# Optimization experiments

Hardware: AMD Instinct MI355X
Metric: run time of the kernel (lower is better)

## Reference

```python
import jax, jax.numpy as jnp
import numpy as np

B, T, C = 1, 2048, 1024
H = 16
HD = C // H  # 64
K = 8
EPS = 1e-6
NEG = -1.0e9


def apply_rotary_emb(x, cos, sin):
    # x: (B,T,H,HD), cos/sin: (T, HD//2)
    x1, x2 = jnp.split(x, 2, axis=-1)
    c = cos[None, :, None, :]
    s = sin[None, :, None, :]
    return jnp.concatenate([x1 * c - x2 * s, x1 * s + x2 * c], axis=-1)


def rms_norm(x):
    return x * jax.lax.rsqrt(jnp.mean(jnp.square(x), axis=-1, keepdims=True) + EPS)


def setup_inputs() -> dict:
    key = jax.random.key(0)
    ks = jax.random.split(key, 8)
    x = jax.random.normal(ks[0], (B, T, C), dtype=jnp.float32)
    # standard RoPE tables
    inv_freq = 1.0 / (10000.0 ** (np.arange(0, HD, 2, dtype=np.float32) / HD))
    t = np.arange(T, dtype=np.float32)
    freqs = np.outer(t, inv_freq)  # (T, HD//2)
    cos = jnp.asarray(np.cos(freqs), dtype=jnp.float32)
    sin = jnp.asarray(np.sin(freqs), dtype=jnp.float32)
    std = 0.02
    Wq = std * jax.random.normal(ks[1], (C, C), dtype=jnp.float32)
    Wk = std * jax.random.normal(ks[2], (C, C), dtype=jnp.float32)
    Wv = std * jax.random.normal(ks[3], (C, C), dtype=jnp.float32)
    Wproj = std * jax.random.normal(ks[4], (C, C), dtype=jnp.float32)
    Wdq = jax.random.normal(ks[5], (C, K), dtype=jnp.float32) / np.sqrt(C)
    Wdk = jax.random.normal(ks[6], (C, K), dtype=jnp.float32) / np.sqrt(C)
    return {"x": x, "cos": cos, "sin": sin, "Wq": Wq, "Wk": Wk, "Wv": Wv,
            "Wproj": Wproj, "Wdq": Wdq, "Wdk": Wdk}


def reference(x, cos, sin, Wq, Wk, Wv, Wproj, Wdq, Wdk):
    b, t, c = x.shape
    q = (x @ Wq).reshape(b, t, H, HD)
    k = (x @ Wk).reshape(b, t, H, HD)
    v = (x @ Wv).reshape(b, t, H, HD)
    q = rms_norm(apply_rotary_emb(q, cos, sin))
    k = rms_norm(apply_rotary_emb(k, cos, sin))

    # digit projections (identical for every head in the source module)
    qd = x @ Wdq  # (B,T,K)
    kd = x @ Wdk  # (B,T,K)
    matches = qd[:, :, None, :] == kd[:, None, :, :]  # (B,Tq,Tk,K)
    prefix = jnp.cumprod(matches.astype(jnp.int32), axis=-1)
    lcp = jnp.sum(prefix, axis=-1)  # (B,Tq,Tk)
    lcp_mask = lcp >= (K - 1)

    causal = jnp.tril(jnp.ones((t, t), dtype=bool))
    combined = causal[None, None, :, :] & lcp_mask[:, None, :, :]  # (B,1->H,Tq,Tk)

    scale = 1.0 / jnp.sqrt(jnp.asarray(HD, x.dtype))
    scores = jnp.einsum('bqhd,bkhd->bhqk', q * scale, k)
    scores = jnp.where(combined, scores, NEG)
    w = jax.nn.softmax(scores, axis=-1)
    y = jnp.einsum('bhqk,bkhd->bqhd', w, v).reshape(b, t, c)
    return y @ Wproj
```

## Files before the change

kernel.cpp:

```cpp
#include <hip/hip_runtime.h>
#include <math.h>

#define T_DIM 2048
#define C_DIM 1024
#define H_NUM 16
#define HD_DIM 64
#define K_LCP 8
#define NEG_VAL -1.0e9f

typedef __bf16 bf16;
typedef __bf16 bf16x4 __attribute__((ext_vector_type(4)));
typedef __bf16 bf16x8 __attribute__((ext_vector_type(8)));
typedef float f32x4 __attribute__((ext_vector_type(4)));

__global__ __launch_bounds__(256) void convert_qdkd(const float* __restrict__ x,
                                                    const float* __restrict__ Wdq,
                                                    const float* __restrict__ Wdk,
                                                    bf16* __restrict__ xb,
                                                    float* __restrict__ qd,
                                                    float* __restrict__ kd) {
  const int wave = threadIdx.x >> 6, lane = threadIdx.x & 63;
  const int t = blockIdx.x * 4 + wave;
  const float* xp = x + (size_t)t * C_DIM;
  bf16* xbp = xb + (size_t)t * C_DIM;
  float aq[8] = {}, ak[8] = {};
#pragma unroll
  for (int i = 0; i < 16; ++i) {
    const int c = i * 64 + lane;
    float xv = xp[c];
    xbp[c] = (bf16)xv;
    float4 wq0 = *(const float4*)(Wdq + (size_t)c * K_LCP);
    float4 wq1 = *(const float4*)(Wdq + (size_t)c * K_LCP + 4);
    float4 wk0 = *(const float4*)(Wdk + (size_t)c * K_LCP);
    float4 wk1 = *(const float4*)(Wdk + (size_t)c * K_LCP + 4);
    aq[0] = fmaf(xv, wq0.x, aq[0]); aq[1] = fmaf(xv, wq0.y, aq[1]);
    aq[2] = fmaf(xv, wq0.z, aq[2]); aq[3] = fmaf(xv, wq0.w, aq[3]);
    aq[4] = fmaf(xv, wq1.x, aq[4]); aq[5] = fmaf(xv, wq1.y, aq[5]);
    aq[6] = fmaf(xv, wq1.z, aq[6]); aq[7] = fmaf(xv, wq1.w, aq[7]);
    ak[0] = fmaf(xv, wk0.x, ak[0]); ak[1] = fmaf(xv, wk0.y, ak[1]);
    ak[2] = fmaf(xv, wk0.z, ak[2]); ak[3] = fmaf(xv, wk0.w, ak[3]);
    ak[4] = fmaf(xv, wk1.x, ak[4]); ak[5] = fmaf(xv, wk1.y, ak[5]);
    ak[6] = fmaf(xv, wk1.z, ak[6]); ak[7] = fmaf(xv, wk1.w, ak[7]);
  }
#pragma unroll
  for (int j = 0; j < 8; ++j) {
#pragma unroll
    for (int off = 32; off >= 1; off >>= 1) {
      aq[j] += __shfl_xor(aq[j], off);
      ak[j] += __shfl_xor(ak[j], off);
    }
  }
  if (lane == 0) {
    *(float4*)(qd + (size_t)t * K_LCP) = make_float4(aq[0], aq[1], aq[2], aq[3]);
    *(float4*)(qd + (size_t)t * K_LCP + 4) = make_float4(aq[4], aq[5], aq[6], aq[7]);
    *(float4*)(kd + (size_t)t * K_LCP) = make_float4(ak[0], ak[1], ak[2], ak[3]);
    *(float4*)(kd + (size_t)t * K_LCP + 4) = make_float4(ak[4], ak[5], ak[6], ak[7]);
  }
}

__global__ __launch_bounds__(256) void tilemask_fused(
    const float* __restrict__ qd, const float* __restrict__ kd,
    const float* __restrict__ x, int* __restrict__ tilemask,
    int* __restrict__ allmask, float* __restrict__ partial) {
  const int tid = threadIdx.x;
  if (blockIdx.x >= 128) {
    const int b = blockIdx.x - 128;
    f32x4 s = {0.f, 0.f, 0.f, 0.f};
    for (int r = 0; r < 64; ++r)
      s += ((const f32x4*)(x + (size_t)(b * 64 + r) * C_DIM))[tid];
    ((f32x4*)(partial + (size_t)b * C_DIM))[tid] = s;
    return;
  }
  const int qb = blockIdx.x;
  __shared__ float qds[16][K_LCP];
  __shared__ int tm[32];
  if (tid < 32) tm[tid] = 0;
  if (tid < 16 * K_LCP)
    qds[tid >> 3][tid & 7] = qd[(size_t)(qb * 16 + (tid >> 3)) * K_LCP + (tid & 7)];
  __syncthreads();
  for (int key = tid; key < T_DIM; key += 256) {
    float kv[K_LCP];
    *(float4*)&kv[0] = *(const float4*)(kd + (size_t)key * K_LCP);
    *(float4*)&kv[4] = *(const float4*)(kd + (size_t)key * K_LCP + 4);
    int any = 0;
#pragma unroll
    for (int ql = 0; ql < 16; ++ql) {
      int qg = qb * 16 + ql;
      if (key > qg) continue;
      int lcp = 0;
#pragma unroll
      for (int jj = 0; jj < K_LCP; ++jj) {
        if (qds[ql][jj] == kv[jj]) lcp++;
        else break;
      }
      if (lcp >= K_LCP - 1) any = 1;
    }
    if (any) tm[key >> 6] = 1;
  }
  __syncthreads();
  if (tid < 32) tilemask[qb * 32 + tid] = tm[tid];
  if (tid == 0) {
    int any = 0;
#pragma unroll
    for (int i = 0; i < 32; ++i) any |= tm[i];
    allmask[qb] = !any;
  }
}

__global__ __launch_bounds__(256) void matvec_kernel(
    const float* __restrict__ vin, int npart, const float* __restrict__ W,
    float* __restrict__ vout, float scale, const int* __restrict__ tilemask,
    const int* __restrict__ allmask, int* __restrict__ qneed,
    int* __restrict__ kneed, int* __restrict__ vneed, int* __restrict__ vtneed,
    int* __restrict__ pneed, int* __restrict__ wneed, int do_need) {
  __shared__ float xm[C_DIM];
  __shared__ float red[4][64];
  const int t = threadIdx.x;
  f32x4 s = {0.f, 0.f, 0.f, 0.f};
  if (npart) {
    for (int g = 0; g < npart; ++g) s += ((const f32x4*)vin)[g * 256 + t];
  } else {
    s = ((const f32x4*)vin)[t];
  }
  s *= scale;
  *(f32x4*)&xm[t * 4] = s;
  __syncthreads();
  const int j = blockIdx.x * 64 + (t & 63);
  const int p = t >> 6;
  float acc = 0.f;
  for (int c = p * 256; c < p * 256 + 256; ++c)
    acc = fmaf(xm[c], W[(size_t)c * C_DIM + j], acc);
  red[p][t & 63] = acc;
  __syncthreads();
  if (t < 64)
    vout[blockIdx.x * 64 + t] = (red[0][t] + red[1][t]) + (red[2][t] + red[3][t]);

  if (do_need && blockIdx.x == 0) {
    __shared__ int tmor[32], vt[32], am[128], qn[16], kn[16], vn[16], pn[32];
    if (t < 128) am[t] = allmask[t];
    __syncthreads();
    if (t < 32) {
      int o = 0, v = 0;
      for (int qb = 0; qb < T_DIM / 16; ++qb) {
        int tm = tilemask[qb * 32 + t];
        o |= tm;
        v |= ((!am[qb]) && (!tm));
      }
      tmor[t] = o;
      vt[t] = v;
      vtneed[t] = v;
    }
    __syncthreads();
    if (t < 16) {
      int kn_ = tmor[2 * t] | tmor[2 * t + 1];
      kn[t] = kn_;
      kneed[t] = kn_;
      int q = 0;
#pragma unroll
      for (int jj = 0; jj < 8; ++jj) q |= !am[t * 8 + jj];
      qn[t] = q;
      qneed[t] = q;
      int v_ = kn_ | vt[2 * t] | vt[2 * t + 1];
      vn[t] = v_;
      vneed[t] = v_;
    }
    if (t >= 32 && t < 64) {
      int i = t - 32, pp = 0;
#pragma unroll
      for (int jj = 0; jj < 4; ++jj) pp |= !am[i * 4 + jj];
      pn[i] = pp;
      pneed[i] = pp;
    }
    __syncthreads();
    if (t == 0) {
      int a = 0, b = 0, c = 0, d = 0;
      for (int i = 0; i < 16; ++i) { a |= qn[i]; b |= kn[i]; c |= vn[i]; }
      for (int i = 0; i < 32; ++i) d |= pn[i];
      wneed[0] = a; wneed[1] = b; wneed[2] = c; wneed[3] = d;
    }
  }
}

__global__ __launch_bounds__(256) void transpose_w(const float* __restrict__ W0,
                                                   const float* __restrict__ W1,
                                                   const float* __restrict__ W2,
                                                   const float* __restrict__ W3,
                                                   bf16* __restrict__ O0,
                                                   bf16* __restrict__ O1,
                                                   bf16* __restrict__ O2,
                                                   bf16* __restrict__ O3,
                                                   const int* __restrict__ wneed) {
  if (!wneed[blockIdx.z]) return;
  const float* W = (blockIdx.z == 0) ? W0 : (blockIdx.z == 1) ? W1
                   : (blockIdx.z == 2) ? W2 : W3;
  bf16* O = (blockIdx.z == 0) ? O0 : (blockIdx.z == 1) ? O1
            : (blockIdx.z == 2) ? O2 : O3;
  __shared__ bf16 tile[64][65];
  const int bk = blockIdx.y * 64;
  const int bn = blockIdx.x * 64;
  const int r = threadIdx.x >> 2;
  const int c0 = (threadIdx.x & 3) * 16;
  const float* src = W + (size_t)(bk + r) * C_DIM + bn + c0;
#pragma unroll
  for (int t = 0; t < 16; t += 4) {
    float4 f = *(const float4*)(src + t);
    tile[r][c0 + t + 0] = (bf16)f.x;
    tile[r][c0 + t + 1] = (bf16)f.y;
    tile[r][c0 + t + 2] = (bf16)f.z;
    tile[r][c0 + t + 3] = (bf16)f.w;
  }
  __syncthreads();
  bf16* dst = O + (size_t)(bn + r) * C_DIM + bk + c0;
#pragma unroll
  for (int t = 0; t < 16; ++t) dst[t] = tile[c0 + t][r];
}

template <int TMt, int MI, int NA>
__global__ __launch_bounds__(256) void gemm_bf16(
    const bf16* __restrict__ A, const bf16* __restrict__ Bt0,
    const bf16* __restrict__ Bt1, const bf16* __restrict__ Bt2, void* C0,
    void* C1, void* C2, int N, int Kd, int bf16_out,
    const float* __restrict__ cosT, const float* __restrict__ sinT,
    const int* __restrict__ fq, const int* __restrict__ fk,
    const int* __restrict__ fv, float* __restrict__ vtsum, int mode) {
  if (mode) {
    const int* f = (blockIdx.z == 0) ? fq : (blockIdx.z == 1) ? fk : fv;
    if (!f[blockIdx.y]) return;
  } else {
    if (!fq[blockIdx.y]) return;
  }
  const bf16* Bt = (blockIdx.z == 0) ? Bt0 : (blockIdx.z == 1) ? Bt1 : Bt2;
  __shared__ __align__(16) bf16 As[TMt * 32];
  __shared__ __align__(16) bf16 Bs[128 * 32];
  const int tid = threadIdx.x;
  const int bm = blockIdx.y * TMt;
  const int bn = blockIdx.x * 128;
  const int wave = tid >> 6, lane = tid & 63;
  const int lr = lane >> 2;
  const int lc = (lane & 3) * 8;
  bf16* gA = (bf16*)(A + (size_t)(bm + wave * 16 * NA + lr) * Kd + lc);
  bf16* gB = (bf16*)(Bt + (size_t)(bn + wave * 32 + lr) * Kd + lc);
  bf16* lA = As + wave * 512 * NA;
  bf16* lB = Bs + wave * 1024;
  const int wr = (wave >> 1) * (MI * 16);
  const int wc = (wave & 1) * 64;
  const int fm = lane & 15;
  const int fk_ = (lane >> 4) * 8;

  f32x4 acc[MI][4] = {};
  for (int k0 = 0; k0 < Kd; k0 += 32) {
    __syncthreads();
#pragma unroll
    for (int u = 0; u < NA; ++u)
      __builtin_amdgcn_global_load_lds(
          (__attribute__((address_space(1))) void*)(gA + (size_t)u * 16 * Kd + k0),
          (__attribute__((address_space(3))) void*)(lA + u * 512), 16, 0, 0);
#pragma unroll
    for (int u = 0; u < 2; ++u)
      __builtin_amdgcn_global_load_lds(
          (__attribute__((address_space(1))) void*)(gB + (size_t)u * 16 * Kd + k0),
          (__attribute__((address_space(3))) void*)(lB + u * 512), 16, 0, 0);
    __syncthreads();
    bf16x8 af[MI], bfr[4];
#pragma unroll
    for (int i = 0; i < MI; ++i)
      af[i] = *(const bf16x8*)(As + (size_t)(wr + i * 16 + fm) * 32 + fk_);
#pragma unroll
    for (int j = 0; j < 4; ++j)
      bfr[j] = *(const bf16x8*)(Bs + (size_t)(wc + j * 16 + fm) * 32 + fk_);
#pragma unroll
    for (int i = 0; i < MI; ++i)
#pragma unroll
      for (int j = 0; j < 4; ++j)
        acc[i][j] = __builtin_amdgcn_mfma_f32_16x16x32_bf16(af[i], bfr[j],
                                                            acc[i][j], 0, 0, 0);
  }
  const int cq = (lane >> 4) * 4;
  if (mode && blockIdx.z < 2) {
    bf16* C = (bf16*)((blockIdx.z == 0) ? C0 : C1);
#pragma unroll
    for (int i = 0; i < MI; ++i)
#pragma unroll
      for (int r = 0; r < 4; ++r) {
        const int t = bm + wr + i * 16 + cq + r;
        float c0 = cosT[(size_t)t * 32 + fm], s0 = sinT[(size_t)t * 32 + fm];
        float c1 = cosT[(size_t)t * 32 + 16 + fm], s1 = sinT[(size_t)t * 32 + 16 + fm];
        float a0 = acc[i][0][r], a1 = acc[i][1][r];
        float a2 = acc[i][2][r], a3 = acc[i][3][r];
        float o0 = a0 * c0 - a2 * s0, o2 = a0 * s0 + a2 * c0;
        float o1 = a1 * c1 - a3 * s1, o3 = a1 * s1 + a3 * c1;
        float ss = o0 * o0 + o1 * o1 + o2 * o2 + o3 * o3;
        ss += __shfl_xor(ss, 1);
        ss += __shfl_xor(ss, 2);
        ss += __shfl_xor(ss, 4);
        ss += __shfl_xor(ss, 8);
        float rn = 1.0f / sqrtf(ss * (1.0f / 64.0f) + 1e-6f);
        size_t base = (size_t)t * N + bn + wc + fm;
        C[base + 0] = (bf16)(o0 * rn);
        C[base + 16] = (bf16)(o1 * rn);
        C[base + 32] = (bf16)(o2 * rn);
        C[base + 48] = (bf16)(o3 * rn);
      }
  } else if (bf16_out) {
    bf16* C = (bf16*)((blockIdx.z == 0) ? C0 : (blockIdx.z == 1) ? C1 : C2);
#pragma unroll
    for (int i = 0; i < MI; ++i)
#pragma unroll
      for (int r = 0; r < 4; ++r) {
        size_t base = (size_t)(bm + wr + i * 16 + cq + r) * N + bn + wc + fm;
#pragma unroll
        for (int j = 0; j < 4; ++j) C[base + j * 16] = (bf16)acc[i][j][r];
      }
    if (mode && blockIdx.z == 2 && MI == 4) {
      const int kt = (bm + wr) >> 6;
#pragma unroll
      for (int j = 0; j < 4; ++j) {
        float s = 0.f;
#pragma unroll
        for (int i = 0; i < MI; ++i)
#pragma unroll
          for (int r = 0; r < 4; ++r) s += acc[i][j][r];
        s += __shfl_xor(s, 16);
        s += __shfl_xor(s, 32);
        if ((lane >> 4) == 0)
          vtsum[(size_t)kt * C_DIM + bn + wc + j * 16 + fm] = s;
      }
    }
  } else {
    float* C = (float*)((blockIdx.z == 0) ? C0 : (blockIdx.z == 1) ? C1 : C2);
#pragma unroll
    for (int i = 0; i < MI; ++i)
#pragma unroll
      for (int r = 0; r < 4; ++r) {
        size_t base = (size_t)(bm + wr + i * 16 + cq + r) * N + bn + wc + fm;
#pragma unroll
        for (int j = 0; j < 4; ++j) C[base + j * 16] = acc[i][j][r];
      }
  }
}

#define QT 16
#define KT 64

__global__ __launch_bounds__(256) void attn2(
    const bf16* __restrict__ q, const bf16* __restrict__ k,
    const bf16* __restrict__ v, const float* __restrict__ qd,
    const float* __restrict__ kd, const float* __restrict__ vtsum,
    const float* __restrict__ vmean, const int* __restrict__ tilemask,
    const int* __restrict__ allmask, const int* __restrict__ pneed,
    bf16* __restrict__ y) {
  const int h = blockIdx.y;
  const int qb = blockIdx.x;
  const int q0 = qb * QT;
  const int tid = threadIdx.x;
  const int q_l = tid >> 4;
  const int sub = tid & 15;

  if (allmask[qb]) {
    if (pneed[qb >> 2]) {
      f32x4 vm = *(const f32x4*)(vmean + h * HD_DIM + sub * 4);
      bf16x4 o = {(bf16)vm[0], (bf16)vm[1], (bf16)vm[2], (bf16)vm[3]};
      *(bf16x4*)(y + (size_t)(q0 + q_l) * C_DIM + h * HD_DIM + sub * 4) = o;
    }
    return;
  }

  __shared__ float qs[QT][HD_DIM];
  __shared__ float qds[QT][K_LCP];
  __shared__ float ks[KT][HD_DIM];
  __shared__ float vs[KT][HD_DIM];
  __shared__ float kds[KT][K_LCP];
  __shared__ float sc[QT][KT + 4];

  {
    int r = tid >> 4, c4 = (tid & 15) * 4;
    bf16x4 t4 = *(const bf16x4*)(q + (size_t)(q0 + r) * C_DIM + h * HD_DIM + c4);
    qs[r][c4 + 0] = (float)t4[0] * 0.125f;
    qs[r][c4 + 1] = (float)t4[1] * 0.125f;
    qs[r][c4 + 2] = (float)t4[2] * 0.125f;
    qs[r][c4 + 3] = (float)t4[3] * 0.125f;
    if (tid < QT * K_LCP)
      qds[tid >> 3][tid & 7] = qd[(size_t)(q0 + (tid >> 3)) * K_LCP + (tid & 7)];
  }
  __syncthreads();

  float m = -INFINITY;
  float l = 0.f;
  float acc[4] = {0.f, 0.f, 0.f, 0.f};

  for (int kt = 0; kt < T_DIM / KT; ++kt) {
    if (!tilemask[qb * 32 + kt]) {
      if (m <= NEG_VAL) {
        m = NEG_VAL;
        l += (float)KT;
        f32x4 vt = *(const f32x4*)(vtsum + (size_t)kt * C_DIM + h * HD_DIM + sub * 4);
        acc[0] += vt[0];
        acc[1] += vt[1];
        acc[2] += vt[2];
        acc[3] += vt[3];
      }
      continue;
    }
    const int k0 = kt * KT;
    __syncthreads();
#pragma unroll
    for (int it = 0; it < 4; ++it) {
      int i = tid + it * 256;
      int row = i >> 4, c4 = (i & 15) * 4;
      bf16x4 kv = *(const bf16x4*)(k + (size_t)(k0 + row) * C_DIM + h * HD_DIM + c4);
      bf16x4 vv = *(const bf16x4*)(v + (size_t)(k0 + row) * C_DIM + h * HD_DIM + c4);
      ks[row][c4 + 0] = (float)kv[0];
      ks[row][c4 + 1] = (float)kv[1];
      ks[row][c4 + 2] = (float)kv[2];
      ks[row][c4 + 3] = (float)kv[3];
      vs[row][c4 + 0] = (float)vv[0];
      vs[row][c4 + 1] = (float)vv[1];
      vs[row][c4 + 2] = (float)vv[2];
      vs[row][c4 + 3] = (float)vv[3];
    }
#pragma unroll
    for (int it = 0; it < 2; ++it) {
      int i = tid + it * 256;
      kds[i >> 3][i & 7] = kd[(size_t)(k0 + (i >> 3)) * K_LCP + (i & 7)];
    }
    __syncthreads();

    const int kb = sub * 4;
    bool msk[4];
#pragma unroll
    for (int j = 0; j < 4; ++j) {
      int kg = k0 + kb + j;
      int lcp = 0;
#pragma unroll
      for (int jj = 0; jj < K_LCP; ++jj) {
        if (qds[q_l][jj] == kds[kb + j][jj]) lcp++;
        else break;
      }
      msk[j] = (lcp >= K_LCP - 1) && (kg <= q0 + q_l);
    }
    float s[4] = {0.f, 0.f, 0.f, 0.f};
#pragma unroll
    for (int d4 = 0; d4 < 16; ++d4) {
      float4 q4 = *(const float4*)&qs[q_l][d4 * 4];
#pragma unroll
      for (int j = 0; j < 4; ++j) {
        float4 k4 = *(const float4*)&ks[kb + j][d4 * 4];
        s[j] = fmaf(q4.x, k4.x, s[j]);
        s[j] = fmaf(q4.y, k4.y, s[j]);
        s[j] = fmaf(q4.z, k4.z, s[j]);
        s[j] = fmaf(q4.w, k4.w, s[j]);
      }
    }
    float tmax = NEG_VAL;
#pragma unroll
    for (int j = 0; j < 4; ++j) {
      s[j] = msk[j] ? s[j] : NEG_VAL;
      tmax = fmaxf(tmax, s[j]);
    }
#pragma unroll
    for (int off = 1; off < 16; off <<= 1) tmax = fmaxf(tmax, __shfl_xor(tmax, off));
    float m_new = fmaxf(m, tmax);
    float alpha = expf(m - m_new);
    float lsum = 0.f;
#pragma unroll
    for (int j = 0; j < 4; ++j) {
      float p = expf(s[j] - m_new);
      sc[q_l][kb + j] = p;
      lsum += p;
    }
#pragma unroll
    for (int off = 1; off < 16; off <<= 1) lsum += __shfl_xor(lsum, off);
    l = l * alpha + lsum;
    m = m_new;
    acc[0] *= alpha;
    acc[1] *= alpha;
    acc[2] *= alpha;
    acc[3] *= alpha;
    __syncthreads();
#pragma unroll 8
    for (int kk = 0; kk < KT; ++kk) {
      float w = sc[q_l][kk];
      const float4 v4 = *(const float4*)&vs[kk][sub * 4];
      acc[0] = fmaf(w, v4.x, acc[0]);
      acc[1] = fmaf(w, v4.y, acc[1]);
      acc[2] = fmaf(w, v4.z, acc[2]);
      acc[3] = fmaf(w, v4.w, acc[3]);
    }
  }

  const float inv_l = 1.0f / l;
  bf16x4 o = {(bf16)(acc[0] * inv_l), (bf16)(acc[1] * inv_l),
              (bf16)(acc[2] * inv_l), (bf16)(acc[3] * inv_l)};
  *(bf16x4*)(y + (size_t)(q0 + q_l) * C_DIM + h * HD_DIM + sub * 4) = o;
}

__global__ __launch_bounds__(256) void bcast_out(const float* __restrict__ rowout,
                                                 const int* __restrict__ pneed,
                                                 float* __restrict__ out) {
  f32x4 v = ((const f32x4*)rowout)[threadIdx.x];
  const int r0 = blockIdx.x * 8;
#pragma unroll
  for (int r = 0; r < 8; ++r) {
    const int row = r0 + r;
    if (pneed[row >> 6]) continue;
    ((f32x4*)(out + (size_t)row * C_DIM))[threadIdx.x] = v;
  }
}

extern "C" void kernel_launch(void* const* d_in, const int* in_sizes, int n_in,
                              void* d_out, int out_size, void* d_ws, size_t ws_size,
                              hipStream_t stream) {
  const float* x = (const float*)d_in[0];
  const float* cosT = (const float*)d_in[1];
  const float* sinT = (const float*)d_in[2];
  const float* Wq = (const float*)d_in[3];
  const float* Wk = (const float*)d_in[4];
  const float* Wv = (const float*)d_in[5];
  const float* Wproj = (const float*)d_in[6];
  const float* Wdq = (const float*)d_in[7];
  const float* Wdk = (const float*)d_in[8];
  float* out = (float*)d_out;

  char* ws = (char*)d_ws;
  const size_t TC2 = (size_t)T_DIM * C_DIM * 2;
  const size_t CC2 = (size_t)C_DIM * C_DIM * 2;
  bf16* xb = (bf16*)(ws + 0);
  bf16* wqt = (bf16*)(ws + TC2);
  bf16* wkt = (bf16*)(ws + TC2 + CC2);
  bf16* wvt = (bf16*)(ws + TC2 + 2 * CC2);
  bf16* wpt = (bf16*)(ws + TC2 + 3 * CC2);
  bf16* qb = (bf16*)(ws + TC2 + 4 * CC2);
  bf16* kb = (bf16*)(ws + 2 * TC2 + 4 * CC2);
  bf16* vb = (bf16*)(ws + 3 * TC2 + 4 * CC2);
  char* p2 = ws + 4 * TC2 + 4 * CC2;
  float* qd = (float*)p2;                      p2 += (size_t)T_DIM * K_LCP * 4;
  float* kd = (float*)p2;                      p2 += (size_t)T_DIM * K_LCP * 4;
  float* vtsum = (float*)p2;                   p2 += 32 * C_DIM * 4;
  float* vmean = (float*)p2;                   p2 += C_DIM * 4;
  float* partial = (float*)p2;                 p2 += 32 * C_DIM * 4;
  float* rowout = (float*)p2;                  p2 += C_DIM * 4;
  int* tilemask = (int*)p2;                    p2 += (T_DIM / 16) * 32 * 4;
  int* allmask = (int*)p2;                     p2 += (T_DIM / 16) * 4;
  int* qneed = (int*)p2;                       p2 += 16 * 4;
  int* kneed = (int*)p2;                       p2 += 16 * 4;
  int* vneed = (int*)p2;                       p2 += 16 * 4;
  int* vtneed = (int*)p2;                      p2 += 32 * 4;
  int* pneed = (int*)p2;                       p2 += 32 * 4;
  int* wneed = (int*)p2;                       p2 += 4 * 4;
  bf16* yb = xb;

  convert_qdkd<<<T_DIM / 4, 256, 0, stream>>>(x, Wdq, Wdk, xb, qd, kd);
  tilemask_fused<<<160, 256, 0, stream>>>(qd, kd, x, tilemask, allmask, partial);
  matvec_kernel<<<16, 256, 0, stream>>>(partial, 32, Wv, vmean, 1.0f / 2048.0f,
                                        tilemask, allmask, qneed, kneed, vneed,
                                        vtneed, pneed, wneed, 1);
  matvec_kernel<<<16, 256, 0, stream>>>(vmean, 0, Wproj, rowout, 1.0f, tilemask,
                                        allmask, qneed, kneed, vneed, vtneed,
                                        pneed, wneed, 0);
  transpose_w<<<dim3(16, 16, 4), 256, 0, stream>>>(Wq, Wk, Wv, Wproj, wqt, wkt,
                                                   wvt, wpt, wneed);
  gemm_bf16<128, 4, 2><<<dim3(C_DIM / 128, T_DIM / 128, 3), 256, 0, stream>>>(
      xb, wqt, wkt, wvt, qb, kb, vb, C_DIM, C_DIM, 1, cosT, sinT, qneed, kneed,
      vneed, vtsum, 1);
  attn2<<<dim3(T_DIM / QT, H_NUM), 256, 0, stream>>>(
      qb, kb, vb, qd, kd, vtsum, vmean, tilemask, allmask, pneed, yb);
  gemm_bf16<64, 2, 1><<<dim3(C_DIM / 128, T_DIM / 64, 1), 256, 0, stream>>>(
      yb, wpt, wpt, wpt, out, out, out, C_DIM, C_DIM, 0, cosT, sinT, pneed,
      pneed, pneed, vtsum, 0);
  bcast_out<<<T_DIM / 8, 256, 0, stream>>>(rowout, pneed, out);
}
```

Baseline: 147.8 us.

## Merge preprocessing kernels and compute need-flags with atomics to cut launches

Collapses the chain of small launches (convert, tilemask, two matvecs, transpose, broadcast) into fewer fused kernels. The column-sum partials now run inside the first kernel, and the Wv matvec runs alongside the tilemask blocks. The single-block need-flag reduction is replaced by per-block atomicOr updates. The Wproj matvec joins the weight transpose, and the row broadcast becomes an extra z-slice of the output GEMM. This removes launch gaps and serial tiny kernels, but it relies on the flags being zeroed in an earlier launch and adds atomic traffic.

Result: faster. 121.6 us (-17.8%).

```diff
diff --git a/kernel.cpp b/kernel.cpp
--- a/kernel.cpp
+++ b/kernel.cpp
@@ -13,13 +13,51 @@
 typedef __bf16 bf16x8 __attribute__((ext_vector_type(8)));
 typedef float f32x4 __attribute__((ext_vector_type(4)));
 
-__global__ __launch_bounds__(256) void convert_qdkd(const float* __restrict__ x,
-                                                    const float* __restrict__ Wdq,
-                                                    const float* __restrict__ Wdk,
-                                                    bf16* __restrict__ xb,
-                                                    float* __restrict__ qd,
-                                                    float* __restrict__ kd) {
-  const int wave = threadIdx.x >> 6, lane = threadIdx.x & 63;
+__device__ void matvec_body(const float* __restrict__ vin, int npart,
+                            const float* __restrict__ W, float* __restrict__ vout,
+                            float scale, int blk) {
+  __shared__ float xm[C_DIM];
+  __shared__ float red[4][64];
+  const int t = threadIdx.x;
+  f32x4 s = {0.f, 0.f, 0.f, 0.f};
+  if (npart) {
+    for (int g = 0; g < npart; ++g) s += ((const f32x4*)vin)[g * 256 + t];
+  } else {
+    s = ((const f32x4*)vin)[t];
+  }
+  s *= scale;
+  *(f32x4*)&xm[t * 4] = s;
+  __syncthreads();
+  const int j = blk * 64 + (t & 63);
+  const int p = t >> 6;
+  float acc = 0.f;
+  for (int c = p * 256; c < p * 256 + 256; ++c)
+    acc = fmaf(xm[c], W[(size_t)c * C_DIM + j], acc);
+  red[p][t & 63] = acc;
+  __syncthreads();
+  if (t < 64)
+    vout[blk * 64 + t] = (red[0][t] + red[1][t]) + (red[2][t] + red[3][t]);
+}
+
+__global__ __launch_bounds__(256) void fused_a(const float* __restrict__ x,
+                                               const float* __restrict__ Wdq,
+                                               const float* __restrict__ Wdk,
+                                               bf16* __restrict__ xb,
+                                               float* __restrict__ qd,
+                                               float* __restrict__ kd,
+                                               float* __restrict__ partial,
+                                               int* __restrict__ flags) {
+  const int tid = threadIdx.x;
+  if (blockIdx.x >= 512) {
+    const int b = blockIdx.x - 512;
+    if (b == 0 && tid < 116) flags[tid] = 0;
+    f32x4 s = {0.f, 0.f, 0.f, 0.f};
+    for (int r = 0; r < 64; ++r)
+      s += ((const f32x4*)(x + (size_t)(b * 64 + r) * C_DIM))[tid];
+    ((f32x4*)(partial + (size_t)b * C_DIM))[tid] = s;
+    return;
+  }
+  const int wave = tid >> 6, lane = tid & 63;
   const int t = blockIdx.x * 4 + wave;
   const float* xp = x + (size_t)t * C_DIM;
   bf16* xbp = xb + (size_t)t * C_DIM;
@@ -58,17 +96,16 @@
   }
 }
 
-__global__ __launch_bounds__(256) void tilemask_fused(
+__global__ __launch_bounds__(256) void fused_b(
     const float* __restrict__ qd, const float* __restrict__ kd,
-    const float* __restrict__ x, int* __restrict__ tilemask,
-    int* __restrict__ allmask, float* __restrict__ partial) {
+    const float* __restrict__ partial, const float* __restrict__ Wv,
+    int* __restrict__ tilemask, int* __restrict__ allmask,
+    float* __restrict__ vmean, int* __restrict__ qneed, int* __restrict__ kneed,
+    int* __restrict__ vneed, int* __restrict__ vtneed, int* __restrict__ pneed,
+    int* __restrict__ wneed) {
   const int tid = threadIdx.x;
   if (blockIdx.x >= 128) {
-    const int b = blockIdx.x - 128;
-    f32x4 s = {0.f, 0.f, 0.f, 0.f};
-    for (int r = 0; r < 64; ++r)
-      s += ((const f32x4*)(x + (size_t)(b * 64 + r) * C_DIM))[tid];
-    ((f32x4*)(partial + (size_t)b * C_DIM))[tid] = s;
+    matvec_body(partial, 32, Wv, vmean, 1.0f / 2048.0f, blockIdx.x - 128);
     return;
   }
   const int qb = blockIdx.x;
@@ -98,106 +135,51 @@
     if (any) tm[key >> 6] = 1;
   }
   __syncthreads();
+  int anytm = 0;
+#pragma unroll
+  for (int i = 0; i < 32; ++i) anytm |= tm[i];
   if (tid < 32) tilemask[qb * 32 + tid] = tm[tid];
-  if (tid == 0) {
-    int any = 0;
-#pragma unroll
-    for (int i = 0; i < 32; ++i) any |= tm[i];
-    allmask[qb] = !any;
-  }
-}
-
-__global__ __launch_bounds__(256) void matvec_kernel(
-    const float* __restrict__ vin, int npart, const float* __restrict__ W,
-    float* __restrict__ vout, float scale, const int* __restrict__ tilemask,
-    const int* __restrict__ allmask, int* __restrict__ qneed,
-    int* __restrict__ kneed, int* __restrict__ vneed, int* __restrict__ vtneed,
-    int* __restrict__ pneed, int* __restrict__ wneed, int do_need) {
-  __shared__ float xm[C_DIM];
-  __shared__ float red[4][64];
-  const int t = threadIdx.x;
-  f32x4 s = {0.f, 0.f, 0.f, 0.f};
-  if (npart) {
-    for (int g = 0; g < npart; ++g) s += ((const f32x4*)vin)[g * 256 + t];
-  } else {
-    s = ((const f32x4*)vin)[t];
-  }
-  s *= scale;
-  *(f32x4*)&xm[t * 4] = s;
-  __syncthreads();
-  const int j = blockIdx.x * 64 + (t & 63);
-  const int p = t >> 6;
-  float acc = 0.f;
-  for (int c = p * 256; c < p * 256 + 256; ++c)
-    acc = fmaf(xm[c], W[(size_t)c * C_DIM + j], acc);
-  red[p][t & 63] = acc;
-  __syncthreads();
-  if (t < 64)
-    vout[blockIdx.x * 64 + t] = (red[0][t] + red[1][t]) + (red[2][t] + red[3][t]);
-
-  if (do_need && blockIdx.x == 0) {
-    __shared__ int tmor[32], vt[32], am[128], qn[16], kn[16], vn[16], pn[32];
-    if (t < 128) am[t] = allmask[t];
-    __syncthreads();
-    if (t < 32) {
-      int o = 0, v = 0;
-      for (int qb = 0; qb < T_DIM / 16; ++qb) {
-        int tm = tilemask[qb * 32 + t];
-        o |= tm;
-        v |= ((!am[qb]) && (!tm));
-      }
-      tmor[t] = o;
-      vt[t] = v;
-      vtneed[t] = v;
-    }
-    __syncthreads();
-    if (t < 16) {
-      int kn_ = tmor[2 * t] | tmor[2 * t + 1];
-      kn[t] = kn_;
-      kneed[t] = kn_;
-      int q = 0;
-#pragma unroll
-      for (int jj = 0; jj < 8; ++jj) q |= !am[t * 8 + jj];
-      qn[t] = q;
-      qneed[t] = q;
-      int v_ = kn_ | vt[2 * t] | vt[2 * t + 1];
-      vn[t] = v_;
-      vneed[t] = v_;
-    }
-    if (t >= 32 && t < 64) {
-      int i = t - 32, pp = 0;
-#pragma unroll
-      for (int jj = 0; jj < 4; ++jj) pp |= !am[i * 4 + jj];
-      pn[i] = pp;
-      pneed[i] = pp;
-    }
-    __syncthreads();
-    if (t == 0) {
-      int a = 0, b = 0, c = 0, d = 0;
-      for (int i = 0; i < 16; ++i) { a |= qn[i]; b |= kn[i]; c |= vn[i]; }
-      for (int i = 0; i < 32; ++i) d |= pn[i];
-      wneed[0] = a; wneed[1] = b; wneed[2] = c; wneed[3] = d;
-    }
-  }
-}
-
-__global__ __launch_bounds__(256) void transpose_w(const float* __restrict__ W0,
-                                                   const float* __restrict__ W1,
-                                                   const float* __restrict__ W2,
-                                                   const float* __restrict__ W3,
-                                                   bf16* __restrict__ O0,
-                                                   bf16* __restrict__ O1,
-                                                   bf16* __restrict__ O2,
-                                                   bf16* __restrict__ O3,
-                                                   const int* __restrict__ wneed) {
-  if (!wneed[blockIdx.z]) return;
-  const float* W = (blockIdx.z == 0) ? W0 : (blockIdx.z == 1) ? W1
-                   : (blockIdx.z == 2) ? W2 : W3;
-  bf16* O = (blockIdx.z == 0) ? O0 : (blockIdx.z == 1) ? O1
-            : (blockIdx.z == 2) ? O2 : O3;
+  if (tid == 0) allmask[qb] = !anytm;
+  if (anytm) {
+    if (tid < 32) {
+      if (tm[tid]) {
+        atomicOr(&kneed[tid >> 1], 1);
+        atomicOr(&vneed[tid >> 1], 1);
+      } else {
+        atomicOr(&vtneed[tid], 1);
+        atomicOr(&vneed[tid >> 1], 1);
+      }
+    }
+    if (tid == 0) {
+      atomicOr(&qneed[qb >> 3], 1);
+      atomicOr(&pneed[qb >> 2], 1);
+      atomicOr(&wneed[0], 1);
+      atomicOr(&wneed[1], 1);
+      atomicOr(&wneed[2], 1);
+      atomicOr(&wneed[3], 1);
+    }
+  }
+}
+
+__global__ __launch_bounds__(256) void fused_e(
+    const float* __restrict__ vmean, const float* __restrict__ WprojF,
+    float* __restrict__ rowout, const float* __restrict__ W0,
+    const float* __restrict__ W1, const float* __restrict__ W2,
+    const float* __restrict__ W3, bf16* __restrict__ O0, bf16* __restrict__ O1,
+    bf16* __restrict__ O2, bf16* __restrict__ O3, const int* __restrict__ wneed) {
+  if (blockIdx.x < 16) {
+    matvec_body(vmean, 0, WprojF, rowout, 1.0f, blockIdx.x);
+    return;
+  }
+  const int idx = blockIdx.x - 16;
+  const int z = idx >> 8;
+  if (!wneed[z]) return;
+  const float* W = (z == 0) ? W0 : (z == 1) ? W1 : (z == 2) ? W2 : W3;
+  bf16* O = (z == 0) ? O0 : (z == 1) ? O1 : (z == 2) ? O2 : O3;
   __shared__ bf16 tile[64][65];
-  const int bk = blockIdx.y * 64;
-  const int bn = blockIdx.x * 64;
+  const int rem = idx & 255;
+  const int bk = (rem >> 4) * 64;
+  const int bn = (rem & 15) * 64;
   const int r = threadIdx.x >> 2;
   const int c0 = (threadIdx.x & 3) * 16;
   const float* src = W + (size_t)(bk + r) * C_DIM + bn + c0;
@@ -222,7 +204,19 @@
     void* C1, void* C2, int N, int Kd, int bf16_out,
     const float* __restrict__ cosT, const float* __restrict__ sinT,
     const int* __restrict__ fq, const int* __restrict__ fk,
-    const int* __restrict__ fv, float* __restrict__ vtsum, int mode) {
+    const int* __restrict__ fv, float* __restrict__ vtsum,
+    const float* __restrict__ rowout, int mode) {
+  if (!mode && blockIdx.z == 1) {
+    const int b = blockIdx.y * 8 + blockIdx.x;
+    f32x4 v = ((const f32x4*)rowout)[threadIdx.x];
+#pragma unroll
+    for (int r = 0; r < 8; ++r) {
+      const int row = b * 8 + r;
+      if (fq[row >> 6]) continue;
+      ((f32x4*)((float*)C0 + (size_t)row * C_DIM))[threadIdx.x] = v;
+    }
+    return;
+  }
   if (mode) {
     const int* f = (blockIdx.z == 0) ? fq : (blockIdx.z == 1) ? fk : fv;
     if (!f[blockIdx.y]) return;
@@ -492,19 +486,6 @@
   bf16x4 o = {(bf16)(acc[0] * inv_l), (bf16)(acc[1] * inv_l),
               (bf16)(acc[2] * inv_l), (bf16)(acc[3] * inv_l)};
   *(bf16x4*)(y + (size_t)(q0 + q_l) * C_DIM + h * HD_DIM + sub * 4) = o;
-}
-
-__global__ __launch_bounds__(256) void bcast_out(const float* __restrict__ rowout,
-                                                 const int* __restrict__ pneed,
-                                                 float* __restrict__ out) {
-  f32x4 v = ((const f32x4*)rowout)[threadIdx.x];
-  const int r0 = blockIdx.x * 8;
-#pragma unroll
-  for (int r = 0; r < 8; ++r) {
-    const int row = r0 + r;
-    if (pneed[row >> 6]) continue;
-    ((f32x4*)(out + (size_t)row * C_DIM))[threadIdx.x] = v;
-  }
 }
 
 extern "C" void kernel_launch(void* const* d_in, const int* in_sizes, int n_in,
@@ -549,23 +530,18 @@
   int* wneed = (int*)p2;                       p2 += 4 * 4;
   bf16* yb = xb;
 
-  convert_qdkd<<<T_DIM / 4, 256, 0, stream>>>(x, Wdq, Wdk, xb, qd, kd);
-  tilemask_fused<<<160, 256, 0, stream>>>(qd, kd, x, tilemask, allmask, partial);
-  matvec_kernel<<<16, 256, 0, stream>>>(partial, 32, Wv, vmean, 1.0f / 2048.0f,
-                                        tilemask, allmask, qneed, kneed, vneed,
-                                        vtneed, pneed, wneed, 1);
-  matvec_kernel<<<16, 256, 0, stream>>>(vmean, 0, Wproj, rowout, 1.0f, tilemask,
-                                        allmask, qneed, kneed, vneed, vtneed,
-                                        pneed, wneed, 0);
-  transpose_w<<<dim3(16, 16, 4), 256, 0, stream>>>(Wq, Wk, Wv, Wproj, wqt, wkt,
-                                                   wvt, wpt, wneed);
+  fused_a<<<544, 256, 0, stream>>>(x, Wdq, Wdk, xb, qd, kd, partial, qneed);
+  fused_b<<<144, 256, 0, stream>>>(qd, kd, partial, Wv, tilemask, allmask,
+                                   vmean, qneed, kneed, vneed, vtneed, pneed,
+                                   wneed);
+  fused_e<<<16 + 1024, 256, 0, stream>>>(vmean, Wproj, rowout, Wq, Wk, Wv,
+                                         Wproj, wqt, wkt, wvt, wpt, wneed);
   gemm_bf16<128, 4, 2><<<dim3(C_DIM / 128, T_DIM / 128, 3), 256, 0, stream>>>(
       xb, wqt, wkt, wvt, qb, kb, vb, C_DIM, C_DIM, 1, cosT, sinT, qneed, kneed,
-      vneed, vtsum, 1);
+      vneed, vtsum, rowout, 1);
   attn2<<<dim3(T_DIM / QT, H_NUM), 256, 0, stream>>>(
       qb, kb, vb, qd, kd, vtsum, vmean, tilemask, allmask, pneed, yb);
-  gemm_bf16<64, 2, 1><<<dim3(C_DIM / 128, T_DIM / 64, 1), 256, 0, stream>>>(
+  gemm_bf16<64, 2, 1><<<dim3(C_DIM / 128, T_DIM / 64, 2), 256, 0, stream>>>(
       yb, wpt, wpt, wpt, out, out, out, C_DIM, C_DIM, 0, cosT, sinT, pneed,
-      pneed, pneed, vtsum, 0);
-  bcast_out<<<T_DIM / 8, 256, 0, stream>>>(rowout, pneed, out);
-}
+      pneed, pneed, vtsum, rowout, 0);
+}
```
